# Performance work log

Hardware: AMD Instinct MI355X
Metric: run time of the kernel (lower is better)

The kernel has to match this reference:

```python
import jax, jax.numpy as jnp
import numpy as np

GRAVITY = 9.81
W_INERTIA = 1.0
W_GRAVITY = 0.01
W_STRAIN = 1.0

V = 500_000
E = 2_000_000


def setup_inputs() -> dict:
    key = jax.random.key(0)
    ks = jax.random.split(key, 7)
    pos_next = jax.random.normal(ks[0], (V, 3), dtype=jnp.float32)
    pos_curr = jax.random.normal(ks[1], (V, 3), dtype=jnp.float32)
    pos_prev = jax.random.normal(ks[2], (V, 3), dtype=jnp.float32)
    mass = jax.random.uniform(ks[3], (V, 1), dtype=jnp.float32)
    elements = jax.random.randint(ks[4], (E, 4), 0, V, dtype=jnp.int64)
    rest_volumes = jax.random.uniform(ks[5], (E,), dtype=jnp.float32)
    rest_inv = jax.random.normal(ks[6], (E, 3, 3), dtype=jnp.float32)
    lam = jnp.float32(1.0)
    mu = jnpp_one = jnp.float32(1.0)
    return {
        "pos_next": pos_next, "pos_curr": pos_curr, "pos_prev": pos_prev,
        "mass": mass, "elements": elements, "rest_volumes": rest_volumes,
        "rest_inv": rest_inv, "lam": lam, "mu": mu,
    }


def _det3(F):
    # F: (E, 3, 3)
    return (F[:, 0, 0] * (F[:, 1, 1] * F[:, 2, 2] - F[:, 1, 2] * F[:, 2, 1])
            - F[:, 0, 1] * (F[:, 1, 0] * F[:, 2, 2] - F[:, 1, 2] * F[:, 2, 0])
            + F[:, 0, 2] * (F[:, 1, 0] * F[:, 2, 1] - F[:, 1, 1] * F[:, 2, 0]))


def _physics_loss(pos_next, pos_curr, pos_prev, mass, elements, rest_volumes, rest_inv, lam, mu):
    # Inertia: mean over all V*3 entries of 0.5 * m * a^2
    accel = pos_next + pos_prev - 2.0 * pos_curr          # (V, 3)
    inertia = 0.5 * jnp.mean(mass * accel * accel)
    # Gravity: -mean(m * g * y)
    gravity = -jnp.mean(mass * GRAVITY * pos_curr[:, 1:2])
    # Strain (Neo-Hookean) on pos_next
    v = pos_next[elements]                                 # (E, 4, 3)
    Ds = jnp.stack([v[:, 1] - v[:, 0], v[:, 2] - v[:, 0], v[:, 3] - v[:, 0]], axis=-1)  # (E,3,3)
    F_def = jnp.einsum('eij,ejk->eik', Ds, rest_inv)       # (E, 3, 3)
    det_F = jnp.maximum(_det3(F_def), 1e-8)
    log_det = jnp.log(det_F)
    tr_FtF = jnp.sum(F_def * F_def, axis=(1, 2))           # trace(F^T F) = ||F||_F^2
    psi = 0.5 * lam * log_det ** 2 - mu * log_det + 0.5 * mu * (tr_FtF - 3.0)
    strain = jnp.mean(psi * rest_volumes)
    return W_INERTIA * inertia + W_GRAVITY * gravity + W_STRAIN * strain


def reference(pos_next, pos_curr, pos_prev, mass, elements, rest_volumes, rest_inv, lam, mu):
    return _physics_loss(pos_next, pos_curr, pos_prev, mass, elements, rest_volumes, rest_inv, lam, mu)
```

## Files before the change

kernel.cpp:

```cpp
#include <hip/hip_runtime.h>


#define GRAVITY_F 9.81f

__device__ __forceinline__ float blockReduceSum(float val) {
    #pragma unroll
    for (int off = 32; off > 0; off >>= 1)
        val += __shfl_down(val, off, 64);
    __shared__ float smem[16];
    const int lane = threadIdx.x & 63;
    const int wave = threadIdx.x >> 6;
    if (lane == 0) smem[wave] = val;
    __syncthreads();
    const int nwaves = (blockDim.x + 63) >> 6;
    val = 0.0f;
    if (wave == 0) {
        if (lane < nwaves) val = smem[lane];
        #pragma unroll
        for (int off = 8; off > 0; off >>= 1)
            val += __shfl_down(val, off, 64);
    }
    return val;
}

__global__ void init_acc_kernel(double* acc) {
    if (threadIdx.x == 0 && blockIdx.x == 0) acc[0] = 0.0;
}

__global__ void vert_kernel(const float* __restrict__ pn,
                            const float* __restrict__ pc,
                            const float* __restrict__ pp,
                            const float* __restrict__ mass,
                            double* __restrict__ acc,
                            int V, float sI, float sG) {
    float local = 0.0f;
    for (int v = blockIdx.x * blockDim.x + threadIdx.x; v < V;
         v += gridDim.x * blockDim.x) {
        const float m  = mass[v];
        const float p0 = pc[3 * v + 0];
        const float y  = pc[3 * v + 1];
        const float p2 = pc[3 * v + 2];
        const float a0 = pn[3 * v + 0] + pp[3 * v + 0] - 2.0f * p0;
        const float a1 = pn[3 * v + 1] + pp[3 * v + 1] - 2.0f * y;
        const float a2 = pn[3 * v + 2] + pp[3 * v + 2] - 2.0f * p2;
        local += sI * (m * (a0 * a0 + a1 * a1 + a2 * a2)) + sG * (m * y);
    }
    const float tot = blockReduceSum(local);
    if (threadIdx.x == 0) atomicAdd(acc, (double)tot);
}

__global__ void elem_kernel(const float* __restrict__ pn,
                            const int*   __restrict__ elems,
                            const float* __restrict__ vols,
                            const float* __restrict__ rinv,
                            const float* __restrict__ lam_p,
                            const float* __restrict__ mu_p,
                            double* __restrict__ acc,
                            int E, float sS) {
    const float lam = lam_p[0];
    const float mu  = mu_p[0];
    float local = 0.0f;
    for (int e = blockIdx.x * blockDim.x + threadIdx.x; e < E;
         e += gridDim.x * blockDim.x) {
        const int4 idx = ((const int4*)elems)[e];
        const float* v0 = pn + 3 * (size_t)idx.x;
        const float* v1 = pn + 3 * (size_t)idx.y;
        const float* v2 = pn + 3 * (size_t)idx.z;
        const float* v3 = pn + 3 * (size_t)idx.w;

        float d[3][3];
        #pragma unroll
        for (int i = 0; i < 3; ++i) {
            const float b = v0[i];
            d[i][0] = v1[i] - b;
            d[i][1] = v2[i] - b;
            d[i][2] = v3[i] - b;
        }

        const float* R = rinv + 9 * (size_t)e;
        float F[3][3];
        #pragma unroll
        for (int i = 0; i < 3; ++i) {
            #pragma unroll
            for (int k = 0; k < 3; ++k) {
                F[i][k] = d[i][0] * R[0 * 3 + k]
                        + d[i][1] * R[1 * 3 + k]
                        + d[i][2] * R[2 * 3 + k];
            }
        }

        const float det = F[0][0] * (F[1][1] * F[2][2] - F[1][2] * F[2][1])
                        - F[0][1] * (F[1][0] * F[2][2] - F[1][2] * F[2][0])
                        + F[0][2] * (F[1][0] * F[2][1] - F[1][1] * F[2][0]);
        const float ld = logf(fmaxf(det, 1e-8f));
        float tr = 0.0f;
        #pragma unroll
        for (int i = 0; i < 3; ++i)
            #pragma unroll
            for (int k = 0; k < 3; ++k)
                tr += F[i][k] * F[i][k];

        const float psi = 0.5f * lam * ld * ld - mu * ld + 0.5f * mu * (tr - 3.0f);
        local += sS * (psi * vols[e]);
    }
    const float tot = blockReduceSum(local);
    if (threadIdx.x == 0) atomicAdd(acc, (double)tot);
}

__global__ void finalize_kernel(const double* __restrict__ acc,
                                float* __restrict__ out) {
    if (threadIdx.x == 0 && blockIdx.x == 0) out[0] = (float)acc[0];
}

extern "C" void kernel_launch(void* const* d_in, const int* in_sizes, int n_in,
                              void* d_out, int out_size, void* d_ws, size_t ws_size,
                              hipStream_t stream) {
    const float* pos_next = (const float*)d_in[0];
    const float* pos_curr = (const float*)d_in[1];
    const float* pos_prev = (const float*)d_in[2];
    const float* mass     = (const float*)d_in[3];
    const int*   elements = (const int*)d_in[4];
    const float* rest_vol = (const float*)d_in[5];
    const float* rest_inv = (const float*)d_in[6];
    const float* lam_p    = (const float*)d_in[7];
    const float* mu_p     = (const float*)d_in[8];
    float* out = (float*)d_out;

    const int V = in_sizes[3];
    const int E = in_sizes[5];

    double* acc = (double*)d_ws;

    const float sI = 0.5f / (3.0f * (float)V);
    const float sG = -0.01f * GRAVITY_F / (float)V;
    const float sS = 1.0f / (float)E;

    init_acc_kernel<<<1, 1, 0, stream>>>(acc);
    {
        const int block = 256;
        int grid = (V + block - 1) / block;
        if (grid > 1024) grid = 1024;
        vert_kernel<<<grid, block, 0, stream>>>(pos_next, pos_curr, pos_prev,
                                                mass, acc, V, sI, sG);
    }
    {
        const int block = 256;
        int grid = (E + block - 1) / block;
        if (grid > 2048) grid = 2048;
        elem_kernel<<<grid, block, 0, stream>>>(pos_next, elements, rest_vol,
                                                rest_inv, lam_p, mu_p, acc, E, sS);
    }
    finalize_kernel<<<1, 1, 0, stream>>>(acc, out);
}
```

Measured before the change: 237.1 us.

## Fuse vertex and element kernels into one launch with per-block partial sums

Merges the vertex and element passes into a single kernel with one thread per item (V+E threads), instead of two grid-stride kernels with capped grids. Each block writes its partial sum to workspace, and a single-block kernel then reduces those partials, replacing the double atomics, the init kernel and the finalize kernel. This removes launches and atomic contention and exposes more parallelism for the gather-heavy element work. In exchange it launches about ten thousand blocks, creates a divergent block at the vertex/element boundary, and adds a serial single-block final reduction.

```diff
diff --git a/kernel.cpp b/kernel.cpp
--- a/kernel.cpp
+++ b/kernel.cpp
@@ -1,5 +1,4 @@
 #include <hip/hip_runtime.h>
-
 
 #define GRAVITY_F 9.81f
 
@@ -23,19 +22,24 @@
     return val;
 }
 
-__global__ void init_acc_kernel(double* acc) {
-    if (threadIdx.x == 0 && blockIdx.x == 0) acc[0] = 0.0;
-}
+__global__ void fused_kernel(const float* __restrict__ pn,
+                             const float* __restrict__ pc,
+                             const float* __restrict__ pp,
+                             const float* __restrict__ mass,
+                             const int*   __restrict__ elems,
+                             const float* __restrict__ vols,
+                             const float* __restrict__ rinv,
+                             const float* __restrict__ lam_p,
+                             const float* __restrict__ mu_p,
+                             float* __restrict__ partials,
+                             double* __restrict__ acc,
+                             int V, int E,
+                             float sI, float sG, float sS) {
+    const int i = blockIdx.x * blockDim.x + threadIdx.x;
+    float local = 0.0f;
 
-__global__ void vert_kernel(const float* __restrict__ pn,
-                            const float* __restrict__ pc,
-                            const float* __restrict__ pp,
-                            const float* __restrict__ mass,
-                            double* __restrict__ acc,
-                            int V, float sI, float sG) {
-    float local = 0.0f;
-    for (int v = blockIdx.x * blockDim.x + threadIdx.x; v < V;
-         v += gridDim.x * blockDim.x) {
+    if (i < V) {
+        const int v = i;
         const float m  = mass[v];
         const float p0 = pc[3 * v + 0];
         const float y  = pc[3 * v + 1];
@@ -43,25 +47,11 @@
         const float a0 = pn[3 * v + 0] + pp[3 * v + 0] - 2.0f * p0;
         const float a1 = pn[3 * v + 1] + pp[3 * v + 1] - 2.0f * y;
         const float a2 = pn[3 * v + 2] + pp[3 * v + 2] - 2.0f * p2;
-        local += sI * (m * (a0 * a0 + a1 * a1 + a2 * a2)) + sG * (m * y);
-    }
-    const float tot = blockReduceSum(local);
-    if (threadIdx.x == 0) atomicAdd(acc, (double)tot);
-}
-
-__global__ void elem_kernel(const float* __restrict__ pn,
-                            const int*   __restrict__ elems,
-                            const float* __restrict__ vols,
-                            const float* __restrict__ rinv,
-                            const float* __restrict__ lam_p,
-                            const float* __restrict__ mu_p,
-                            double* __restrict__ acc,
-                            int E, float sS) {
-    const float lam = lam_p[0];
-    const float mu  = mu_p[0];
-    float local = 0.0f;
-    for (int e = blockIdx.x * blockDim.x + threadIdx.x; e < E;
-         e += gridDim.x * blockDim.x) {
+        local = sI * (m * (a0 * a0 + a1 * a1 + a2 * a2)) + sG * (m * y);
+    } else if (i < V + E) {
+        const int e = i - V;
+        const float lam = lam_p[0];
+        const float mu  = mu_p[0];
         const int4 idx = ((const int4*)elems)[e];
         const float* v0 = pn + 3 * (size_t)idx.x;
         const float* v1 = pn + 3 * (size_t)idx.y;
@@ -70,22 +60,22 @@
 
         float d[3][3];
         #pragma unroll
-        for (int i = 0; i < 3; ++i) {
-            const float b = v0[i];
-            d[i][0] = v1[i] - b;
-            d[i][1] = v2[i] - b;
-            d[i][2] = v3[i] - b;
+        for (int r = 0; r < 3; ++r) {
+            const float b = v0[r];
+            d[r][0] = v1[r] - b;
+            d[r][1] = v2[r] - b;
+            d[r][2] = v3[r] - b;
         }
 
         const float* R = rinv + 9 * (size_t)e;
         float F[3][3];
         #pragma unroll
-        for (int i = 0; i < 3; ++i) {
+        for (int r = 0; r < 3; ++r) {
             #pragma unroll
             for (int k = 0; k < 3; ++k) {
-                F[i][k] = d[i][0] * R[0 * 3 + k]
-                        + d[i][1] * R[1 * 3 + k]
-                        + d[i][2] * R[2 * 3 + k];
+                F[r][k] = d[r][0] * R[0 * 3 + k]
+                        + d[r][1] * R[1 * 3 + k]
+                        + d[r][2] * R[2 * 3 + k];
             }
         }
 
@@ -95,18 +85,41 @@
         const float ld = logf(fmaxf(det, 1e-8f));
         float tr = 0.0f;
         #pragma unroll
-        for (int i = 0; i < 3; ++i)
+        for (int r = 0; r < 3; ++r)
             #pragma unroll
             for (int k = 0; k < 3; ++k)
-                tr += F[i][k] * F[i][k];
+                tr += F[r][k] * F[r][k];
 
         const float psi = 0.5f * lam * ld * ld - mu * ld + 0.5f * mu * (tr - 3.0f);
-        local += sS * (psi * vols[e]);
+        local = sS * (psi * vols[e]);
     }
+
     const float tot = blockReduceSum(local);
-    if (threadIdx.x == 0) atomicAdd(acc, (double)tot);
+    if (threadIdx.x == 0) {
+        if (partials) partials[blockIdx.x] = tot;
+        else atomicAdd(acc, (double)tot);
+    }
 }
 
+__global__ void reduce_kernel(const float* __restrict__ partials, int n,
+                              float* __restrict__ out) {
+    double s = 0.0;
+    for (int i = threadIdx.x; i < n; i += blockDim.x)
+        s += (double)partials[i];
+    __shared__ double sm[256];
+    sm[threadIdx.x] = s;
+    __syncthreads();
+    #pragma unroll
+    for (int off = 128; off > 0; off >>= 1) {
+        if (threadIdx.x < off) sm[threadIdx.x] += sm[threadIdx.x + off];
+        __syncthreads();
+    }
+    if (threadIdx.x == 0) out[0] = (float)sm[0];
+}
+
+__global__ void init_acc_kernel(double* acc) {
+    if (threadIdx.x == 0 && blockIdx.x == 0) acc[0] = 0.0;
+}
 __global__ void finalize_kernel(const double* __restrict__ acc,
                                 float* __restrict__ out) {
     if (threadIdx.x == 0 && blockIdx.x == 0) out[0] = (float)acc[0];
@@ -129,26 +142,32 @@
     const int V = in_sizes[3];
     const int E = in_sizes[5];
 
-    double* acc = (double*)d_ws;
-
     const float sI = 0.5f / (3.0f * (float)V);
     const float sG = -0.01f * GRAVITY_F / (float)V;
     const float sS = 1.0f / (float)E;
 
-    init_acc_kernel<<<1, 1, 0, stream>>>(acc);
-    {
-        const int block = 256;
-        int grid = (V + block - 1) / block;
-        if (grid > 1024) grid = 1024;
-        vert_kernel<<<grid, block, 0, stream>>>(pos_next, pos_curr, pos_prev,
-                                                mass, acc, V, sI, sG);
+    const int block = 256;
+    const int nitems = V + E;
+    const int grid = (nitems + block - 1) / block;
+
+    const bool use_partials = ws_size >= (size_t)grid * sizeof(float) + 64;
+
+    if (use_partials) {
+        float* partials = (float*)d_ws;
+        fused_kernel<<<grid, block, 0, stream>>>(pos_next, pos_curr, pos_prev,
+                                                 mass, elements, rest_vol,
+                                                 rest_inv, lam_p, mu_p,
+                                                 partials, nullptr,
+                                                 V, E, sI, sG, sS);
+        reduce_kernel<<<1, 256, 0, stream>>>(partials, grid, out);
+    } else {
+        double* acc = (double*)d_ws;
+        init_acc_kernel<<<1, 1, 0, stream>>>(acc);
+        fused_kernel<<<grid, block, 0, stream>>>(pos_next, pos_curr, pos_prev,
+                                                 mass, elements, rest_vol,
+                                                 rest_inv, lam_p, mu_p,
+                                                 nullptr, acc,
+                                                 V, E, sI, sG, sS);
+        finalize_kernel<<<1, 1, 0, stream>>>(acc, out);
     }
-    {
-        const int block = 256;
-        int grid = (E + block - 1) / block;
-        if (grid > 2048) grid = 2048;
-        elem_kernel<<<grid, block, 0, stream>>>(pos_next, elements, rest_vol,
-                                                rest_inv, lam_p, mu_p, acc, E, sS);
-    }
-    finalize_kernel<<<1, 1, 0, stream>>>(acc, out);
 }
```

New measurement: 229.9 us. -3.0%, faster.
